# Kernel optimization log

Hardware: AMD Instinct MI355X
Metric: run time of the kernel (lower is better)

## Reference

```python
import jax, jax.numpy as jnp
import numpy as np


def setup_inputs() -> dict:
    key = jax.random.key(0)
    k1, k2, k3, k4 = jax.random.split(key, 4)
    B, S, IN, OUT, K = 4, 2048, 4096, 4096, 256
    x = jax.random.normal(k1, (B, S, IN), dtype=jnp.float32)
    centroids = jax.random.normal(k2, (K,), dtype=jnp.float32)
    bias = jax.random.normal(k3, (OUT,), dtype=jnp.float32)
    indices = jax.random.randint(k4, (OUT, IN), 0, K, dtype=jnp.int64)
    return {"x": x, "centroids": centroids, "bias": bias, "indices": indices}


def reference(x, centroids, bias, indices):
    # Reconstruct the weight matrix from the codebook: [out, in]
    weight = centroids[indices]
    # F.linear: y = x @ weight.T + bias
    out = jnp.einsum('bsi,oi->bso', x, weight) + bias
    return out
```

## Files before the change

kernel.cpp:

```cpp
#include <hip/hip_runtime.h>
#include <hip/hip_bf16.h>
#include <stdint.h>


typedef unsigned short u16;
typedef __attribute__((ext_vector_type(8))) short short8;
typedef __attribute__((ext_vector_type(8))) u16   u16x8;
typedef __attribute__((ext_vector_type(4))) float f32x4;
typedef __attribute__((ext_vector_type(4))) int   i32x4;

constexpr int Mdim = 8192;
constexpr int Ndim = 4096;
constexpr int Kdim = 4096;

__device__ __forceinline__ u16 f2bf(float f) {
  union { float f; uint32_t u; } v; v.f = f;
  uint32_t u = v.u;
  return (u16)((u + 0x7fffu + ((u >> 16) & 1u)) >> 16);
}

__global__ void decode_weight_kernel(const int* __restrict__ idx,
                                     const float* __restrict__ cent,
                                     u16* __restrict__ wb) {
  __shared__ u16 lut[256];
  const int t = threadIdx.x;
  if (t < 256) lut[t] = f2bf(cent[t]);
  __syncthreads();
  const size_t base = ((size_t)blockIdx.x * 256 + t) * 8;
  i32x4 i0 = *(const i32x4*)(idx + base);
  i32x4 i1 = *(const i32x4*)(idx + base + 4);
  u16x8 r;
  r[0] = lut[i0[0] & 255]; r[1] = lut[i0[1] & 255];
  r[2] = lut[i0[2] & 255]; r[3] = lut[i0[3] & 255];
  r[4] = lut[i1[0] & 255]; r[5] = lut[i1[1] & 255];
  r[6] = lut[i1[2] & 255]; r[7] = lut[i1[3] & 255];
  *(u16x8*)(wb + base) = r;
}

__global__ void cvt_x_kernel(const float* __restrict__ x, u16* __restrict__ xb) {
  const size_t base = ((size_t)blockIdx.x * 256 + threadIdx.x) * 8;
  f32x4 a = *(const f32x4*)(x + base);
  f32x4 b = *(const f32x4*)(x + base + 4);
  u16x8 r;
  r[0] = f2bf(a[0]); r[1] = f2bf(a[1]); r[2] = f2bf(a[2]); r[3] = f2bf(a[3]);
  r[4] = f2bf(b[0]); r[5] = f2bf(b[1]); r[6] = f2bf(b[2]); r[7] = f2bf(b[3]);
  *(u16x8*)(xb + base) = r;
}

__device__ __forceinline__ void async16(const u16* g, u16* l) {
  __builtin_amdgcn_global_load_lds(
      (const __attribute__((address_space(1))) void*)g,
      (__attribute__((address_space(3))) void*)l,
      16, 0, 0);
}

#define BAR() __builtin_amdgcn_s_barrier()
#define LGKM0() do { asm volatile("s_waitcnt lgkmcnt(0)" ::: "memory"); \
                     __builtin_amdgcn_sched_barrier(0); } while (0)
#define VMC4() asm volatile("s_waitcnt vmcnt(4)" ::: "memory")
#define VMC0() asm volatile("s_waitcnt vmcnt(0)" ::: "memory")

__global__ __launch_bounds__(512, 2)
void gemm_bf16_kernel(const u16* __restrict__ A,
                      const u16* __restrict__ B,
                      const float* __restrict__ bias,
                      float* __restrict__ C) {
  __shared__ u16 AsF[32768];
  __shared__ u16 BsF[32768];

  const int t    = threadIdx.x;
  const int lane = t & 63;
  const int w    = t >> 6;
  const int wm   = w >> 2;
  const int wn   = w & 3;
  const int fr   = lane & 15;
  const int fq   = lane >> 4;
  const int cswz = (fr & 6) << 2;

  const int bid = blockIdx.x;
  const int swz = (bid & 7) * 64 + (bid >> 3);
  const int m0 = (swz >> 4) * 256;
  const int n0 = (swz & 15) * 256;

  const int c0   = w * 64 + lane;
  const int r16s = (c0 & 63) >> 2;
  const int srow = ((c0 >> 7) << 4) + r16s;
  const int scol = ((c0 >> 6) & 1) * 32 + (((c0 & 3) * 8) ^ ((r16s & 6) << 2));
  const u16* pA = A + (size_t)(m0 + srow) * Kdim + scol;
  const u16* pB = B + (size_t)(n0 + srow) * Kdim + scol;
  const int dsto = c0 * 8;

  const int aoff = wm * 8192 + fr * 32 + ((fq * 8) ^ cswz);
  const int boff = (wn >> 1) * 8192 + (wn & 1) * 4096 + fr * 32 + ((fq * 8) ^ cswz);

  f32x4 acc[8][4] = {};
  short8 bf[2][4];
  short8 af[2][2];

  auto stageA = [&](int tk, int h) {
    const u16* s = pA + (size_t)h * (128 * Kdim) + tk * 64;
    u16* d = &AsF[((tk & 1) * 2 + h) * 8192 + dsto];
    async16(s, d);
    async16(s + (size_t)(64 * Kdim), d + 4096);
  };
  auto stageB = [&](int tk, int h) {
    const u16* s = pB + (size_t)h * (128 * Kdim) + tk * 64;
    u16* d = &BsF[((tk & 1) * 2 + h) * 8192 + dsto];
    async16(s, d);
    async16(s + (size_t)(64 * Kdim), d + 4096);
  };
  auto rdB = [&](int BUF) {
#pragma unroll
    for (int kk = 0; kk < 2; ++kk)
#pragma unroll
      for (int ni = 0; ni < 4; ++ni)
        bf[kk][ni] = *(const short8*)&BsF[BUF * 16384 + boff + (ni * 2 + kk) * 512];
  };
  auto rdA = [&](int BUF, int q) {
#pragma unroll
    for (int kk = 0; kk < 2; ++kk)
#pragma unroll
      for (int i = 0; i < 2; ++i)
        af[kk][i] = *(const short8*)&AsF[BUF * 16384 + aoff + ((q * 2 + i) * 2 + kk) * 512];
  };
  auto mfmaQ = [&](int q) {
    __builtin_amdgcn_s_setprio(1);
#pragma unroll
    for (int kk = 0; kk < 2; ++kk)
#pragma unroll
      for (int i = 0; i < 2; ++i)
#pragma unroll
        for (int ni = 0; ni < 4; ++ni)
          acc[q * 2 + i][ni] = __builtin_amdgcn_mfma_f32_16x16x32_bf16(
              af[kk][i], bf[kk][ni], acc[q * 2 + i][ni], 0, 0, 0);
    __builtin_amdgcn_s_setprio(0);
  };

#define KT(TK, BUF, DOA, DOB, WAITK)                                    \
  {                                                                     \
    rdB(BUF); rdA(BUF, 0);                                              \
    if (DOA) stageA((TK) + 1, 0);                                       \
    BAR(); LGKM0(); mfmaQ(0); BAR();                                    \
    rdA(BUF, 1);                                                        \
    if (DOA) stageA((TK) + 1, 1);                                       \
    if (DOB) stageB((TK) + 2, 0);                                       \
    BAR(); LGKM0(); mfmaQ(1); BAR();                                    \
    rdA(BUF, 2);                                                        \
    if (DOB) stageB((TK) + 2, 1);                                       \
    BAR(); LGKM0(); mfmaQ(2); BAR();                                    \
    rdA(BUF, 3);                                                        \
    BAR(); LGKM0(); mfmaQ(3);                                           \
    if ((WAITK) == 0) { VMC4(); } else if ((WAITK) == 1) { VMC0(); }    \
    BAR();                                                              \
  }

  stageA(0, 0); stageA(0, 1); stageB(0, 0); stageB(0, 1);
  stageB(1, 0); stageB(1, 1);
  VMC4();
  BAR();

  for (int t2 = 0; t2 < 31; ++t2) {
    const int k0 = 2 * t2;
    KT(k0,     0, 1, 1, 0);
    KT(k0 + 1, 1, 1, 1, 0);
  }
  KT(62, 0, 1, 0, 1);
  KT(63, 1, 0, 0, 2);

  float bv[4];
#pragma unroll
  for (int ni = 0; ni < 4; ++ni)
    bv[ni] = bias[n0 + wn * 64 + ni * 16 + fr];

#pragma unroll
  for (int mi = 0; mi < 8; ++mi) {
#pragma unroll
    for (int j = 0; j < 4; ++j) {
      const int row = m0 + wm * 128 + mi * 16 + fq * 4 + j;
      float* cp = C + (size_t)row * Ndim + n0 + wn * 64 + fr;
#pragma unroll
      for (int ni = 0; ni < 4; ++ni)
        cp[ni * 16] = acc[mi][ni][j] + bv[ni];
    }
  }
}

extern "C" void kernel_launch(void* const* d_in, const int* in_sizes, int n_in,
                              void* d_out, int out_size, void* d_ws, size_t ws_size,
                              hipStream_t stream) {
  const float* x    = (const float*)d_in[0];
  const float* cent = (const float*)d_in[1];
  const float* bias = (const float*)d_in[2];
  const int*   idx  = (const int*)d_in[3];
  float* out = (float*)d_out;

  u16* wb = (u16*)d_ws;
  u16* xb = (u16*)((char*)d_ws + (size_t)Ndim * Kdim * sizeof(u16));

  decode_weight_kernel<<<(Ndim * Kdim) / (256 * 8), 256, 0, stream>>>(idx, cent, wb);
  cvt_x_kernel<<<((size_t)Mdim * Kdim) / (256 * 8), 256, 0, stream>>>(x, xb);

  gemm_bf16_kernel<<<dim3(512), 512, 0, stream>>>(xb, wb, bias, out);
}
```

Baseline: 288.6 us.

## Double-buffer A fragments and prefetch next tile's LDS reads during last MFMA quarter

Splits the A-fragment registers into two ping-pong sets so the LDS reads for the next quarter are issued before the current quarter's MFMAs, waiting with a partial lgkmcnt instead of a full drain. The B fragments and first A quarter of the next K-tile are read from LDS while the final quarter's MFMAs run. The aim is to hide LDS read latency behind matrix math. It costs extra VGPRs, which could cause spills at the two-waves-per-SIMD launch bound, and the sched_barrier was removed from the wait macro, so the compiler may reorder instructions around the waits.

```diff
diff --git a/kernel.cpp b/kernel.cpp
--- a/kernel.cpp
+++ b/kernel.cpp
@@ -54,11 +54,11 @@
       16, 0, 0);
 }
 
-#define BAR() __builtin_amdgcn_s_barrier()
-#define LGKM0() do { asm volatile("s_waitcnt lgkmcnt(0)" ::: "memory"); \
-                     __builtin_amdgcn_sched_barrier(0); } while (0)
-#define VMC4() asm volatile("s_waitcnt vmcnt(4)" ::: "memory")
-#define VMC0() asm volatile("s_waitcnt vmcnt(0)" ::: "memory")
+#define BAR()   __builtin_amdgcn_s_barrier()
+#define LGKM0() asm volatile("s_waitcnt lgkmcnt(0)" ::: "memory")
+#define LGKM4() asm volatile("s_waitcnt lgkmcnt(4)" ::: "memory")
+#define VMC4()  asm volatile("s_waitcnt vmcnt(4)" ::: "memory")
+#define VMC0()  asm volatile("s_waitcnt vmcnt(0)" ::: "memory")
 
 __global__ __launch_bounds__(512, 2)
 void gemm_bf16_kernel(const u16* __restrict__ A,
@@ -95,7 +95,8 @@
 
   f32x4 acc[8][4] = {};
   short8 bf[2][4];
-  short8 af[2][2];
+  short8 afA[2][2];
+  short8 afB[2][2];
 
   auto stageA = [&](int tk, int h) {
     const u16* s = pA + (size_t)h * (128 * Kdim) + tk * 64;
@@ -109,21 +110,26 @@
     async16(s, d);
     async16(s + (size_t)(64 * Kdim), d + 4096);
   };
-  auto rdB = [&](int BUF) {
-#pragma unroll
-    for (int kk = 0; kk < 2; ++kk)
-#pragma unroll
-      for (int ni = 0; ni < 4; ++ni)
-        bf[kk][ni] = *(const short8*)&BsF[BUF * 16384 + boff + (ni * 2 + kk) * 512];
-  };
-  auto rdA = [&](int BUF, int q) {
-#pragma unroll
-    for (int kk = 0; kk < 2; ++kk)
-#pragma unroll
-      for (int i = 0; i < 2; ++i)
-        af[kk][i] = *(const short8*)&AsF[BUF * 16384 + aoff + ((q * 2 + i) * 2 + kk) * 512];
-  };
-  auto mfmaQ = [&](int q) {
+  auto rdB_kk = [&](int BUF, int kk) {
+#pragma unroll
+    for (int ni = 0; ni < 4; ++ni)
+      bf[kk][ni] = *(const short8*)&BsF[BUF * 16384 + boff + (ni * 2 + kk) * 512];
+  };
+  auto rdA_A = [&](int BUF, int q) {
+#pragma unroll
+    for (int kk = 0; kk < 2; ++kk)
+#pragma unroll
+      for (int i = 0; i < 2; ++i)
+        afA[kk][i] = *(const short8*)&AsF[BUF * 16384 + aoff + ((q * 2 + i) * 2 + kk) * 512];
+  };
+  auto rdA_B = [&](int BUF, int q) {
+#pragma unroll
+    for (int kk = 0; kk < 2; ++kk)
+#pragma unroll
+      for (int i = 0; i < 2; ++i)
+        afB[kk][i] = *(const short8*)&AsF[BUF * 16384 + aoff + ((q * 2 + i) * 2 + kk) * 512];
+  };
+  auto mfmaE = [&](int q) {
     __builtin_amdgcn_s_setprio(1);
 #pragma unroll
     for (int kk = 0; kk < 2; ++kk)
@@ -132,25 +138,61 @@
 #pragma unroll
         for (int ni = 0; ni < 4; ++ni)
           acc[q * 2 + i][ni] = __builtin_amdgcn_mfma_f32_16x16x32_bf16(
-              af[kk][i], bf[kk][ni], acc[q * 2 + i][ni], 0, 0, 0);
+              afA[kk][i], bf[kk][ni], acc[q * 2 + i][ni], 0, 0, 0);
     __builtin_amdgcn_s_setprio(0);
   };
-
-#define KT(TK, BUF, DOA, DOB, WAITK)                                    \
+  auto mfmaO = [&](int q) {
+    __builtin_amdgcn_s_setprio(1);
+#pragma unroll
+    for (int kk = 0; kk < 2; ++kk)
+#pragma unroll
+      for (int i = 0; i < 2; ++i)
+#pragma unroll
+        for (int ni = 0; ni < 4; ++ni)
+          acc[q * 2 + i][ni] = __builtin_amdgcn_mfma_f32_16x16x32_bf16(
+              afB[kk][i], bf[kk][ni], acc[q * 2 + i][ni], 0, 0, 0);
+    __builtin_amdgcn_s_setprio(0);
+  };
+  auto mfmaO_kk = [&](int q, int kk) {
+    __builtin_amdgcn_s_setprio(1);
+#pragma unroll
+    for (int i = 0; i < 2; ++i)
+#pragma unroll
+      for (int ni = 0; ni < 4; ++ni)
+        acc[q * 2 + i][ni] = __builtin_amdgcn_mfma_f32_16x16x32_bf16(
+            afB[kk][i], bf[kk][ni], acc[q * 2 + i][ni], 0, 0, 0);
+    __builtin_amdgcn_s_setprio(0);
+  };
+
+#define KT(TK, BUF, DOA, DOB, MODE)                                     \
   {                                                                     \
-    rdB(BUF); rdA(BUF, 0);                                              \
+                                                                \
+    rdA_B((BUF), 1);                                                    \
     if (DOA) stageA((TK) + 1, 0);                                       \
-    BAR(); LGKM0(); mfmaQ(0); BAR();                                    \
-    rdA(BUF, 1);                                                        \
+    BAR(); LGKM4();            \
+    mfmaE(0);                                                           \
+    BAR();                                                              \
+                                                                \
+    rdA_A((BUF), 2);                                                    \
     if (DOA) stageA((TK) + 1, 1);                                       \
     if (DOB) stageB((TK) + 2, 0);                                       \
-    BAR(); LGKM0(); mfmaQ(1); BAR();                                    \
-    rdA(BUF, 2);                                                        \
+    BAR(); LGKM4();                                   \
+    mfmaO(1);                                                           \
+    BAR();                                                              \
+                                                                \
+    rdA_B((BUF), 3);                                                    \
     if (DOB) stageB((TK) + 2, 1);                                       \
-    BAR(); LGKM0(); mfmaQ(2); BAR();                                    \
-    rdA(BUF, 3);                                                        \
-    BAR(); LGKM0(); mfmaQ(3);                                           \
-    if ((WAITK) == 0) { VMC4(); } else if ((WAITK) == 1) { VMC0(); }    \
+    BAR(); LGKM4();                                   \
+    mfmaE(2);                                                           \
+    BAR();                                                              \
+                                                      \
+    if ((MODE) == 0) { VMC4(); } else if ((MODE) == 1) { VMC0(); }      \
+    BAR();                         \
+    LGKM0();                                          \
+    mfmaO_kk(3, 0);                                                     \
+    if ((MODE) < 2) rdB_kk((BUF) ^ 1, 0);                               \
+    mfmaO_kk(3, 1);                                                     \
+    if ((MODE) < 2) { rdB_kk((BUF) ^ 1, 1); rdA_A((BUF) ^ 1, 0); }      \
     BAR();                                                              \
   }
 
@@ -158,6 +200,7 @@
   stageB(1, 0); stageB(1, 1);
   VMC4();
   BAR();
+  rdB_kk(0, 0); rdB_kk(0, 1); rdA_A(0, 0);
 
   for (int t2 = 0; t2 < 31; ++t2) {
     const int k0 = 2 * t2;
@@ -183,6 +226,7 @@
         cp[ni * 16] = acc[mi][ni][j] + bv[ni];
     }
   }
+#undef KT
 }
 
 extern "C" void kernel_launch(void* const* d_in, const int* in_sizes, int n_in,
```

Measured after the change: 285.0 us. About the same (-1.2%).
